# Performance work log

Measured on AMD Instinct MI355X. Metric: run time of the kernel, lower is better.

## Reference

```python
import jax, jax.numpy as jnp
import numpy as np

B, L, D, H = 2, 4096, 1024, 4
DK = D // H
DV = D // H
CHUNK, FIRS, FIRL, CONV, GROUP = 32, 3, 31, 4, 2
EPS_ID, R_EPS = 0.06, 0.025   # step==0 -> router epsilon at its start value
R_HID = 2 * D
R_IN = D + H * 6


def _l2norm(x, eps=1e-6):
    return x * jax.lax.rsqrt(jnp.sum(x * x, -1, keepdims=True) + eps)


def _causal_dwconv(x, w):
    # x: (b, l, c), w: (c, k); depthwise causal conv1d
    c = x.shape[-1]
    k = w.shape[-1]
    lhs = jnp.swapaxes(x, 1, 2)              # (b, c, l)
    rhs = w[:, None, :]                      # (c, 1, k)
    y = jax.lax.conv_general_dilated(lhs, rhs, window_strides=(1,), padding=[(k - 1, 0)],
                                     dimension_numbers=('NCH', 'OIH', 'NCH'), feature_group_count=c)
    return jnp.swapaxes(y, 1, 2)


def _fir(x, filt):
    # x: (b, l, h, d), filt: (h, d, k) depthwise causal FIR per head-channel
    b, l, h, d = x.shape
    y = _causal_dwconv(x.reshape(b, l, h * d), filt.reshape(h * d, -1))
    return y.reshape(b, l, h, d)


def _delta_rule_chunkwise(q, k, v, beta, chunk=CHUNK):
    # q,k: (b,h,L,dk)  v: (b,h,L,dv)  beta: (b,h,L); L % chunk == 0
    b, h, Ls, dk = q.shape
    dv = v.shape[-1]
    n = Ls // chunk
    q = _l2norm(q)
    k = _l2norm(k)
    v = v * beta[..., None]
    kb = k * beta[..., None]
    rs = lambda t: t.reshape(b, h, n, chunk, -1)
    q, k, v, kb = map(rs, (q, k, v, kb))
    tri = jnp.triu(jnp.ones((chunk, chunk), bool), 0)
    # UT transform: forward substitution to invert (I + strictly-lower(K_beta K^T))
    T = jnp.where(tri, 0.0, -(kb @ jnp.swapaxes(k, -1, -2)))
    for i in range(1, chunk):
        T = T.at[..., i, :].add(jnp.einsum('...j,...jl->...l', T[..., i, :], T))
    T = T + jnp.eye(chunk, dtype=T.dtype)
    u = T @ v          # (b,h,n,c,dv)
    w = T @ kb         # (b,h,n,c,dk)
    fmask = jnp.triu(jnp.ones((chunk, chunk), bool), 1)
    mv = lambda t: jnp.moveaxis(t, 2, 0)

    def step(S, xs):
        qi, ki, ui, wi = xs
        attn = jnp.where(fmask, 0.0, qi @ jnp.swapaxes(ki, -1, -2))
        u2 = ui - wi @ S
        oi = qi @ S + attn @ u2
        return S + jnp.swapaxes(ki, -1, -2) @ u2, oi

    S0 = jnp.zeros((b, h, dk, dv), q.dtype)
    S, o = jax.lax.scan(step, S0, (mv(q), mv(k), mv(u), mv(w)))
    return jnp.moveaxis(o, 0, 2).reshape(b, h, Ls, dv), S


def setup_inputs():
    key = jax.random.key(0)
    ks = jax.random.split(key, 20)
    lin = lambda kk, i, o: 0.02 * jax.random.normal(kk, (i, o), jnp.float32)

    def fir(kk, kern):
        base = jnp.zeros((H, DV, kern), jnp.float32).at[:, :, -1].set(1.0)
        return base + 0.01 * jax.random.normal(kk, (H, DV, kern), jnp.float32)

    return {
        'hidden_states': jax.random.normal(ks[0], (B, L, D), jnp.float32),
        'Wq': lin(ks[1], D, H * DK), 'Wk': lin(ks[2], D, H * DK), 'Wv': lin(ks[3], D, H * DV),
        'Wb': lin(ks[4], D, H),
        'conv_q': 0.3 * jax.random.normal(ks[5], (H * DK, CONV), jnp.float32),
        'conv_k': 0.3 * jax.random.normal(ks[6], (H * DK, CONV), jnp.float32),
        'conv_v': 0.3 * jax.random.normal(ks[7], (H * DV, CONV), jnp.float32),
        'fir_short': fir(ks[8], FIRS), 'fir_long': fir(ks[9], FIRL),
        'alpha_id': jnp.zeros((H,), jnp.float32),
        'Wid': lin(ks[10], D, H), 'bid': jnp.zeros((H,), jnp.float32),
        'Wr1': lin(ks[11], R_IN, R_HID), 'br1': jnp.zeros((R_HID,), jnp.float32),
        'Wr2': lin(ks[12], R_HID, H * 3), 'br2': jnp.zeros((H * 3,), jnp.float32),
        'log_tau_group': jnp.zeros(((H + GROUP - 1) // GROUP,), jnp.float32),
        'log_tau_head': jnp.zeros((H,), jnp.float32),
        'o_norm_w': jnp.ones((DV,), jnp.float32),
        'Wo': lin(ks[13], H * DV, D),
    }


def reference(hidden_states, Wq, Wk, Wv, Wb, conv_q, conv_k, conv_v, fir_short, fir_long,
              alpha_id, Wid, bid, Wr1, br1, Wr2, br2, log_tau_group, log_tau_head, o_norm_w, Wo):
    x = hidden_states
    b, l = x.shape[:2]
    # projections + causal short conv + silu (qk_activation='silu')
    q = jax.nn.silu(_causal_dwconv(x @ Wq, conv_q))
    k = jax.nn.silu(_causal_dwconv(x @ Wk, conv_k))
    v = jax.nn.silu(_causal_dwconv(x @ Wv, conv_v))
    qh = q.reshape(b, l, H, DK)
    kh = k.reshape(b, l, H, DK)
    vh = v.reshape(b, l, H, DV)
    beta = jax.nn.sigmoid(x @ Wb)                      # (b,l,h)
    bhld = lambda t: jnp.transpose(t, (0, 2, 1, 3))
    delta, _S = _delta_rule_chunkwise(bhld(qh), bhld(kh), bhld(vh), jnp.transpose(beta, (0, 2, 1)))
    delta = jnp.transpose(delta, (0, 2, 1, 3))         # (b,l,h,dv)
    fs = _fir(vh, fir_short)
    fl = _fir(vh, fir_long)
    # per-head mean/std stats of the three branch outputs
    stats = jnp.concatenate([fs.mean(-1), fs.std(-1), fl.mean(-1), fl.std(-1),
                             delta.mean(-1), delta.std(-1)], -1)   # (b,l,6h)
    router_in = jnp.concatenate([x, stats], -1)
    hmid = jax.nn.gelu(router_in @ Wr1 + br1, approximate=False)
    logits = (hmid @ Wr2 + br2).reshape(b, l, H, 3)
    group_idx = jnp.arange(H) // GROUP
    # step==0 -> mix=1.0: tau is the per-group temperature
    tau = jnp.exp(log_tau_group)[group_idx] + 0.0 * jnp.exp(log_tau_head)
    p = jax.nn.softmax(logits / tau[None, None, :, None], -1)
    p = p * (1.0 - 3.0 * R_EPS) + R_EPS                # epsilon-floor
    o = p[..., 0:1] * fs + p[..., 1:2] * fl + p[..., 2:3] * delta
    # gated identity (value) path
    id_scale = EPS_ID + jax.nn.sigmoid(alpha_id)[None, None, :] * jax.nn.sigmoid(x @ Wid + bid)
    o = o + id_scale[..., None] * vh
    # per-head RMSNorm then output projection
    o = o * jax.lax.rsqrt(jnp.mean(o * o, -1, keepdims=True) + 1e-5) * o_norm_w
    return o.reshape(b, l, H * DV) @ Wo
```

## Files before the change

### kernel.cpp

```cpp
#include <hip/hip_runtime.h>
#include <hip/hip_bf16.h>
#include <math.h>

#define BATCH 2
#define SEQ 4096
#define DMODEL 1024
#define NH 4
#define DHEAD 256
#define NCHUNK 128
#define ROWS (BATCH * SEQ)

typedef short s8v __attribute__((ext_vector_type(8)));
typedef float f4v __attribute__((ext_vector_type(4)));

__device__ __forceinline__ float sigm(float x) { return 1.0f / (1.0f + expf(-x)); }
__device__ __forceinline__ float siluf(float x) { return x / (1.0f + expf(-x)); }
__device__ __forceinline__ unsigned short f2b(float f) {
  __hip_bfloat16 h = __float2bfloat16(f);
  return *(unsigned short*)&h;
}
__device__ __forceinline__ float b2f(unsigned short u) {
  __hip_bfloat16 h = *(__hip_bfloat16*)&u;
  return __bfloat162float(h);
}
__device__ __forceinline__ unsigned int pk2(float lo, float hi) {
  return (unsigned int)f2b(lo) | ((unsigned int)f2b(hi) << 16);
}
__device__ __forceinline__ void gload16(const short* g, short* l) {
  __builtin_amdgcn_global_load_lds(
      (const __attribute__((address_space(1))) unsigned int*)(const void*)g,
      (__attribute__((address_space(3))) unsigned int*)(void*)l, 16, 0, 0);
}


__device__ __forceinline__ void prep_body(
    const float* __restrict__ x, __hip_bfloat16* __restrict__ xb,
    const float* __restrict__ Wb, const float* __restrict__ Wid,
    const float* __restrict__ alpha_id, const float* __restrict__ bidp,
    float* __restrict__ beta, float* __restrict__ idsc, int row,
    float (*red)[8]) {
  const int t = threadIdx.x;
  const long base = (long)row * DMODEL + t * 4;
  float4 xv = *(const float4*)(x + base);
  {
    __hip_bfloat16 tmp[4] = {__float2bfloat16(xv.x), __float2bfloat16(xv.y),
                             __float2bfloat16(xv.z), __float2bfloat16(xv.w)};
    *(ushort4*)(xb + base) = *(ushort4*)tmp;
  }
  float xa[4] = {xv.x, xv.y, xv.z, xv.w};
  float ab[4] = {0, 0, 0, 0}, ai[4] = {0, 0, 0, 0};
#pragma unroll
  for (int i = 0; i < 4; ++i) {
    int k = t * 4 + i;
    float4 wb4 = *(const float4*)(Wb + k * 4);
    float4 wi4 = *(const float4*)(Wid + k * 4);
    ab[0] = fmaf(xa[i], wb4.x, ab[0]); ab[1] = fmaf(xa[i], wb4.y, ab[1]);
    ab[2] = fmaf(xa[i], wb4.z, ab[2]); ab[3] = fmaf(xa[i], wb4.w, ab[3]);
    ai[0] = fmaf(xa[i], wi4.x, ai[0]); ai[1] = fmaf(xa[i], wi4.y, ai[1]);
    ai[2] = fmaf(xa[i], wi4.z, ai[2]); ai[3] = fmaf(xa[i], wi4.w, ai[3]);
  }
#pragma unroll
  for (int m = 1; m < 64; m <<= 1) {
#pragma unroll
    for (int hh = 0; hh < 4; ++hh) {
      ab[hh] += __shfl_xor(ab[hh], m);
      ai[hh] += __shfl_xor(ai[hh], m);
    }
  }
  if ((t & 63) == 0) {
    int wv = t >> 6;
#pragma unroll
    for (int hh = 0; hh < 4; ++hh) {
      red[wv][hh] = ab[hh];
      red[wv][4 + hh] = ai[hh];
    }
  }
  __syncthreads();
  if (t < 8) {
    float s = red[0][t] + red[1][t] + red[2][t] + red[3][t];
    if (t < 4) {
      beta[(long)row * NH + t] = sigm(s);
    } else {
      int hh = t - 4;
      idsc[(long)row * NH + hh] = 0.06f + sigm(alpha_id[hh]) * sigm(s + bidp[hh]);
    }
  }
}

__device__ __forceinline__ void tcast_body(
    const float* __restrict__ W, __hip_bfloat16* __restrict__ Wt,
    int K, int N, int Ks, int bx, int by, float (*tile)[33]) {
  const int t = threadIdx.x;
  const int tx = t & 31, ty = t >> 5;
  const int kb = by * 32, nb = bx * 32;
#pragma unroll
  for (int r = 0; r < 4; ++r) {
    int kk = kb + ty + 8 * r;
    tile[ty + 8 * r][tx] = (kk < K) ? W[(long)kk * N + nb + tx] : 0.f;
  }
  __syncthreads();
#pragma unroll
  for (int r = 0; r < 4; ++r) {
    Wt[(long)(nb + ty + 8 * r) * Ks + kb + tx] = __float2bfloat16(tile[tx][ty + 8 * r]);
  }
}

__device__ __forceinline__ void firT_body(
    const float* __restrict__ fshort, const float* __restrict__ flong,
    float* __restrict__ fsT, float* __restrict__ flT, int j) {
  const int t = threadIdx.x;
  if (j < 31) {
#pragma unroll
    for (int i = 0; i < 4; ++i) {
      int c = t * 4 + i;
      flT[j * 1024 + c] = flong[c * 31 + j];
    }
  } else {
    int tp = j - 31;
#pragma unroll
    for (int i = 0; i < 4; ++i) {
      int c = t * 4 + i;
      fsT[tp * 1024 + c] = fshort[c * 3 + tp];
    }
  }
}

__device__ __forceinline__ void stats_body(
    const float* __restrict__ x, const float* __restrict__ fs,
    const float* __restrict__ fl, const float* __restrict__ dl,
    __hip_bfloat16* __restrict__ rinb, int row) {
  const int b = row >> 12;
  const int l = row & (SEQ - 1);
  const int t = threadIdx.x;
  float4 xv = *(const float4*)(x + (long)row * DMODEL + t * 4);
  {
    __hip_bfloat16 tmp[4] = {__float2bfloat16(xv.x), __float2bfloat16(xv.y),
                             __float2bfloat16(xv.z), __float2bfloat16(xv.w)};
    *(ushort4*)(rinb + (long)row * 1056 + t * 4) = *(ushort4*)tmp;
  }
  if (t < 8) rinb[(long)row * 1056 + 1048 + t] = __float2bfloat16(0.f);
  const int h = t >> 6;
  const int lane = t & 63;
  const long base = (long)row * DMODEL + h * DHEAD + lane * 4;
  const long dbase = ((long)(b * NH + h) * SEQ + l) * DHEAD + lane * 4;
  float4 a = *(const float4*)(fs + base);
  float4 bq = *(const float4*)(fl + base);
  float4 cq = *(const float4*)(dl + dbase);
  float s[6];
  s[0] = a.x + a.y + a.z + a.w;
  s[1] = a.x * a.x + a.y * a.y + a.z * a.z + a.w * a.w;
  s[2] = bq.x + bq.y + bq.z + bq.w;
  s[3] = bq.x * bq.x + bq.y * bq.y + bq.z * bq.z + bq.w * bq.w;
  s[4] = cq.x + cq.y + cq.z + cq.w;
  s[5] = cq.x * cq.x + cq.y * cq.y + cq.z * cq.z + cq.w * cq.w;
#pragma unroll
  for (int m = 1; m < 64; m <<= 1)
#pragma unroll
    for (int j = 0; j < 6; ++j) s[j] += __shfl_xor(s[j], m);
  if (lane == 0) {
    __hip_bfloat16* rb = rinb + (long)row * 1056 + 1024;
    float m0 = s[0] * (1.f / 256.f);
    float m1 = s[2] * (1.f / 256.f);
    float m2 = s[4] * (1.f / 256.f);
    rb[h] = __float2bfloat16(m0);
    rb[4 + h] = __float2bfloat16(sqrtf(fmaxf(s[1] * (1.f / 256.f) - m0 * m0, 0.f)));
    rb[8 + h] = __float2bfloat16(m1);
    rb[12 + h] = __float2bfloat16(sqrtf(fmaxf(s[3] * (1.f / 256.f) - m1 * m1, 0.f)));
    rb[16 + h] = __float2bfloat16(m2);
    rb[20 + h] = __float2bfloat16(sqrtf(fmaxf(s[5] * (1.f / 256.f) - m2 * m2, 0.f)));
  }
}


__global__ __launch_bounds__(256) void head_fused(
    const float* __restrict__ x, __hip_bfloat16* __restrict__ xb,
    const float* __restrict__ Wb, const float* __restrict__ Wid,
    const float* __restrict__ alpha_id, const float* __restrict__ bidp,
    float* __restrict__ beta, float* __restrict__ idsc,
    const float* __restrict__ Wq, __hip_bfloat16* __restrict__ Wqt,
    const float* __restrict__ Wk, __hip_bfloat16* __restrict__ Wkt,
    const float* __restrict__ Wv, __hip_bfloat16* __restrict__ Wvt,
    const float* __restrict__ fir_s, const float* __restrict__ fir_l,
    float* __restrict__ fsT, float* __restrict__ flT) {
  __shared__ float tile[32][33];
  __shared__ float red[4][8];
  const int bid = blockIdx.x;
  if (bid < 8192) {
    prep_body(x, xb, Wb, Wid, alpha_id, bidp, beta, idsc, bid, red);
  } else if (bid < 9216) {
    int r = bid - 8192;
    tcast_body(Wq, Wqt, 1024, 1024, 1024, r & 31, r >> 5, tile);
  } else if (bid < 10240) {
    int r = bid - 9216;
    tcast_body(Wk, Wkt, 1024, 1024, 1024, r & 31, r >> 5, tile);
  } else if (bid < 11264) {
    int r = bid - 10240;
    tcast_body(Wv, Wvt, 1024, 1024, 1024, r & 31, r >> 5, tile);
  } else {
    firT_body(fir_s, fir_l, fsT, flT, bid - 11264);
  }
}

__global__ __launch_bounds__(256) void stats_tcast(
    const float* __restrict__ x, const float* __restrict__ fs,
    const float* __restrict__ fl, const float* __restrict__ dl,
    __hip_bfloat16* __restrict__ rinb,
    const float* __restrict__ Wr1, __hip_bfloat16* __restrict__ Wr1t,
    const float* __restrict__ Wo, __hip_bfloat16* __restrict__ Wot) {
  __shared__ float tile[32][33];
  const int bid = blockIdx.x;
  if (bid < 8192) {
    stats_body(x, fs, fl, dl, rinb, bid);
  } else if (bid < 10304) {
    int r = bid - 8192;
    tcast_body(Wr1, Wr1t, 1048, 2048, 1056, r & 63, r >> 6, tile);
  } else {
    int r = bid - 10304;
    tcast_body(Wo, Wot, 1024, 1024, 1024, r & 31, r >> 5, tile);
  }
}

template <int ACT, bool BF16OUT>
__global__ __launch_bounds__(256) void gemm_bf16(
    const __hip_bfloat16* __restrict__ A, const __hip_bfloat16* __restrict__ Bt,
    const float* __restrict__ bias, void* __restrict__ Cv,
    int M, int N, int Ks) {
  __shared__ short As[128 * 32];
  __shared__ short Bs[128 * 32];
  const int t = threadIdx.x;
  const int wv = t >> 6;
  const int lane = t & 63;
  const int row0 = blockIdx.y * 128, col0 = blockIdx.x * 128;
  const int mq = (wv >> 1) * 64, nq = (wv & 1) * 64;
  const int ln15 = lane & 15;
  const int kq = (lane >> 4) * 8;
  const int srow = wv * 16 + (lane >> 2);
  const int scol = (lane & 3) * 8;
  const short* Ag0 = (const short*)A + (long)(row0 + srow) * Ks + scol;
  const short* Ag1 = Ag0 + (long)64 * Ks;
  const short* Bg0 = (const short*)Bt + (long)(col0 + srow) * Ks + scol;
  const short* Bg1 = Bg0 + (long)64 * Ks;
  short* Ad0 = &As[(wv * 16) * 32];
  short* Ad1 = &As[(64 + wv * 16) * 32];
  short* Bd0 = &Bs[(wv * 16) * 32];
  short* Bd1 = &Bs[(64 + wv * 16) * 32];

  f4v acc[4][4];
#pragma unroll
  for (int i = 0; i < 4; ++i)
#pragma unroll
    for (int j = 0; j < 4; ++j) acc[i][j] = (f4v){0.f, 0.f, 0.f, 0.f};

  for (int k0 = 0; k0 < Ks; k0 += 32) {
    __syncthreads();
    gload16(Ag0 + k0, Ad0);
    gload16(Ag1 + k0, Ad1);
    gload16(Bg0 + k0, Bd0);
    gload16(Bg1 + k0, Bd1);
    __syncthreads();
    s8v af[4], bf[4];
#pragma unroll
    for (int mt = 0; mt < 4; ++mt)
      af[mt] = *(const s8v*)&As[(mq + mt * 16 + ln15) * 32 + kq];
#pragma unroll
    for (int nt = 0; nt < 4; ++nt)
      bf[nt] = *(const s8v*)&Bs[(nq + nt * 16 + ln15) * 32 + kq];
#pragma unroll
    for (int mt = 0; mt < 4; ++mt)
#pragma unroll
      for (int nt = 0; nt < 4; ++nt)
        acc[mt][nt] = __builtin_amdgcn_mfma_f32_16x16x32_bf16(af[mt], bf[nt], acc[mt][nt], 0, 0, 0);
  }
  const int rbase = (lane >> 4) * 4;
#pragma unroll
  for (int mt = 0; mt < 4; ++mt) {
#pragma unroll
    for (int nt = 0; nt < 4; ++nt) {
      int gcol = col0 + nq + nt * 16 + ln15;
#pragma unroll
      for (int r = 0; r < 4; ++r) {
        int grow = row0 + mq + mt * 16 + rbase + r;
        float v = acc[mt][nt][r];
        if (ACT == 1) {
          v += bias[gcol];
          v = 0.5f * v * (1.0f + erff(v * 0.70710678118654752f));
        }
        if (BF16OUT) {
          ((__hip_bfloat16*)Cv)[(long)grow * N + gcol] = __float2bfloat16(v);
        } else {
          ((float*)Cv)[(long)grow * N + gcol] = v;
        }
      }
    }
  }
}

template <int MODE>
__global__ __launch_bounds__(256) void conv_silu(
    const float* __restrict__ pre, const float* __restrict__ cw, float* __restrict__ out) {
  const int row = blockIdx.x;
  const int l = row & (SEQ - 1);
  const int t = threadIdx.x;
  const int cb = t * 4;
  float wts[4][4];
#pragma unroll
  for (int cc = 0; cc < 4; ++cc) {
    float4 w4 = *(const float4*)(cw + (cb + cc) * 4);
    wts[cc][0] = w4.x; wts[cc][1] = w4.y; wts[cc][2] = w4.z; wts[cc][3] = w4.w;
  }
  float acc[4] = {0, 0, 0, 0};
#pragma unroll
  for (int tap = 0; tap < 4; ++tap) {
    int lr = l - 3 + tap;
    if (lr >= 0) {
      float4 xv = *(const float4*)(pre + (long)(row - 3 + tap) * DMODEL + cb);
      acc[0] = fmaf(wts[0][tap], xv.x, acc[0]);
      acc[1] = fmaf(wts[1][tap], xv.y, acc[1]);
      acc[2] = fmaf(wts[2][tap], xv.z, acc[2]);
      acc[3] = fmaf(wts[3][tap], xv.w, acc[3]);
    }
  }
#pragma unroll
  for (int i = 0; i < 4; ++i) acc[i] = siluf(acc[i]);
  if (MODE == 1) {
    float ss = acc[0] * acc[0] + acc[1] * acc[1] + acc[2] * acc[2] + acc[3] * acc[3];
#pragma unroll
    for (int m = 1; m < 64; m <<= 1) ss += __shfl_xor(ss, m);
    float rn = rsqrtf(ss + 1e-6f);
#pragma unroll
    for (int i = 0; i < 4; ++i) acc[i] *= rn;
  }
  float4 ov = make_float4(acc[0], acc[1], acc[2], acc[3]);
  *(float4*)(out + (long)row * DMODEL + cb) = ov;
}

__global__ __launch_bounds__(256) void phaseA(
    const float* __restrict__ qn, const float* __restrict__ kn, const float* __restrict__ v,
    const float* __restrict__ beta, float* __restrict__ u,
    __hip_bfloat16* __restrict__ wb16, __hip_bfloat16* __restrict__ kTb16,
    __hip_bfloat16* __restrict__ attnb16, __hip_bfloat16* __restrict__ qpk) {
  __shared__ short khi[32 * 264];
  __shared__ short klo[32 * 264];
  __shared__ float T[32][33];
  __shared__ float bet[32];
  const int bid = blockIdx.x;
  const int c = bid & (NCHUNK - 1);
  const int h = (bid >> 7) & 3;
  const int b = bid >> 9;
  const int bh = b * NH + h;
  const int l0 = c * 32;
  const int t = threadIdx.x;
  const int wv = t >> 6;
  const int lane = t & 63;
  const int ln15 = lane & 15;
  const int qw = lane >> 4;

#pragma unroll
  for (int r = 0; r < 8; ++r) {
    int idx = t + 256 * r;
    int i = idx >> 6;
    int f = (idx & 63) * 4;
    float4 kv = *(const float4*)(kn + ((long)(b * SEQ + l0 + i)) * DMODEL + h * DHEAD + f);
    float a[4] = {kv.x, kv.y, kv.z, kv.w};
    ushort4 hi4, lo4;
    unsigned short* hp = (unsigned short*)&hi4;
    unsigned short* lp = (unsigned short*)&lo4;
#pragma unroll
    for (int j = 0; j < 4; ++j) {
      unsigned short hb = f2b(a[j]);
      hp[j] = hb;
      lp[j] = f2b(a[j] - b2f(hb));
    }
    *(ushort4*)&khi[i * 264 + f] = hi4;
    *(ushort4*)&klo[i * 264 + f] = lo4;
  }
  if (t < 32) bet[t] = beta[(long)(b * SEQ + l0 + t) * NH + h];
  __syncthreads();

  if (wv < 2) {
    const int mt = wv;
    f4v acc0 = (f4v){0.f, 0.f, 0.f, 0.f};
    f4v acc1 = (f4v){0.f, 0.f, 0.f, 0.f};
#pragma unroll
    for (int ks = 0; ks < 8; ++ks) {
      s8v ahi = *(const s8v*)&khi[(mt * 16 + ln15) * 264 + ks * 32 + qw * 8];
      s8v alo = *(const s8v*)&klo[(mt * 16 + ln15) * 264 + ks * 32 + qw * 8];
      s8v bhi0 = *(const s8v*)&khi[ln15 * 264 + ks * 32 + qw * 8];
      s8v blo0 = *(const s8v*)&klo[ln15 * 264 + ks * 32 + qw * 8];
      s8v bhi1 = *(const s8v*)&khi[(16 + ln15) * 264 + ks * 32 + qw * 8];
      s8v blo1 = *(const s8v*)&klo[(16 + ln15) * 264 + ks * 32 + qw * 8];
      acc0 = __builtin_amdgcn_mfma_f32_16x16x32_bf16(ahi, bhi0, acc0, 0, 0, 0);
      acc0 = __builtin_amdgcn_mfma_f32_16x16x32_bf16(ahi, blo0, acc0, 0, 0, 0);
      acc0 = __builtin_amdgcn_mfma_f32_16x16x32_bf16(alo, bhi0, acc0, 0, 0, 0);
      acc1 = __builtin_amdgcn_mfma_f32_16x16x32_bf16(ahi, bhi1, acc1, 0, 0, 0);
      acc1 = __builtin_amdgcn_mfma_f32_16x16x32_bf16(ahi, blo1, acc1, 0, 0, 0);
      acc1 = __builtin_amdgcn_mfma_f32_16x16x32_bf16(alo, bhi1, acc1, 0, 0, 0);
    }
#pragma unroll
    for (int r = 0; r < 4; ++r) {
      int i = mt * 16 + qw * 4 + r;
      int j0 = ln15, j1 = 16 + ln15;
      T[i][j0] = (j0 < i) ? -bet[i] * acc0[r] : 0.f;
      T[i][j1] = (j1 < i) ? -bet[i] * acc1[r] : 0.f;
    }
  } else {
    const int mt = wv - 2;
    const long qoff = (long)(b * SEQ + l0 + mt * 16 + ln15) * DMODEL + h * DHEAD;
    __hip_bfloat16* qdst = qpk + ((long)bh * SEQ + l0 + mt * 16 + ln15) * DHEAD;
    f4v acc0 = (f4v){0.f, 0.f, 0.f, 0.f};
    f4v acc1 = (f4v){0.f, 0.f, 0.f, 0.f};
#pragma unroll
    for (int ks = 0; ks < 8; ++ks) {
      float4 q0 = *(const float4*)(qn + qoff + ks * 32 + qw * 8);
      float4 q1 = *(const float4*)(qn + qoff + ks * 32 + qw * 8 + 4);
      float a8[8] = {q0.x, q0.y, q0.z, q0.w, q1.x, q1.y, q1.z, q1.w};
      s8v ahi, alo;
#pragma unroll
      for (int j = 0; j < 8; ++j) {
        unsigned short hb = f2b(a8[j]);
        ahi[j] = (short)hb;
        alo[j] = (short)f2b(a8[j] - b2f(hb));
      }
      *(s8v*)(qdst + ks * 32 + qw * 8) = ahi;
      s8v bhi0 = *(const s8v*)&khi[ln15 * 264 + ks * 32 + qw * 8];
      s8v blo0 = *(const s8v*)&klo[ln15 * 264 + ks * 32 + qw * 8];
      s8v bhi1 = *(const s8v*)&khi[(16 + ln15) * 264 + ks * 32 + qw * 8];
      s8v blo1 = *(const s8v*)&klo[(16 + ln15) * 264 + ks * 32 + qw * 8];
      acc0 = __builtin_amdgcn_mfma_f32_16x16x32_bf16(ahi, bhi0, acc0, 0, 0, 0);
      acc0 = __builtin_amdgcn_mfma_f32_16x16x32_bf16(ahi, blo0, acc0, 0, 0, 0);
      acc0 = __builtin_amdgcn_mfma_f32_16x16x32_bf16(alo, bhi0, acc0, 0, 0, 0);
      acc1 = __builtin_amdgcn_mfma_f32_16x16x32_bf16(ahi, bhi1, acc1, 0, 0, 0);
      acc1 = __builtin_amdgcn_mfma_f32_16x16x32_bf16(ahi, blo1, acc1, 0, 0, 0);
      acc1 = __builtin_amdgcn_mfma_f32_16x16x32_bf16(alo, bhi1, acc1, 0, 0, 0);
    }
    long abase = ((long)bh * NCHUNK + c) * 1024;
#pragma unroll
    for (int r = 0; r < 4; ++r) {
      int i = mt * 16 + qw * 4 + r;
      int j0 = ln15, j1 = 16 + ln15;
      attnb16[abase + i * 32 + j0] = __float2bfloat16(j0 <= i ? acc0[r] : 0.f);
      attnb16[abase + i * 32 + j1] = __float2bfloat16(j1 <= i ? acc1[r] : 0.f);
    }
  }
  __syncthreads();

  if (t < 32) {
    const int l = t;
    for (int i = 1; i < 32; ++i) {
      float s = 0.f;
      for (int j = 0; j < i; ++j) s = fmaf(T[i][j], T[j][l], s);
      T[i][l] += s;
    }
    for (int i = 0; i < 32; ++i) {
      float val = T[i][l] + (i == l ? 1.f : 0.f);
      T[i][l] = val * bet[l];
    }
  }
  __syncthreads();

  {
    const int d = t;
    float acc[32];
#pragma unroll
    for (int i = 0; i < 32; ++i) acc[i] = 0.f;
    for (int j = 0; j < 32; ++j) {
      float vv = v[((long)(b * SEQ + l0 + j)) * DMODEL + h * DHEAD + d];
#pragma unroll
      for (int i = 0; i < 32; ++i) acc[i] = fmaf(T[i][j], vv, acc[i]);
    }
    long ubase = ((long)bh * SEQ + l0) * DHEAD + d;
#pragma unroll
    for (int i = 0; i < 32; ++i) u[ubase + (long)i * DHEAD] = acc[i];
#pragma unroll
    for (int i = 0; i < 32; ++i) acc[i] = 0.f;
    for (int j = 0; j < 32; ++j) {
      float kv = b2f((unsigned short)khi[j * 264 + d]) + b2f((unsigned short)klo[j * 264 + d]);
#pragma unroll
      for (int i = 0; i < 32; ++i) acc[i] = fmaf(T[i][j], kv, acc[i]);
    }
#pragma unroll
    for (int i = 0; i < 32; ++i) wb16[ubase + (long)i * DHEAD] = __float2bfloat16(acc[i]);
  }

  {
    const int s = t;
    unsigned short* kb = (unsigned short*)kTb16 + ((long)bh * NCHUNK + c) * 8192 + (long)s * 32;
#pragma unroll
    for (int i4 = 0; i4 < 8; ++i4) {
      ushort4 pk;
      pk.x = (unsigned short)khi[(i4 * 4 + 0) * 264 + s];
      pk.y = (unsigned short)khi[(i4 * 4 + 1) * 264 + s];
      pk.z = (unsigned short)khi[(i4 * 4 + 2) * 264 + s];
      pk.w = (unsigned short)khi[(i4 * 4 + 3) * 264 + s];
      *(ushort4*)(kb + i4 * 4) = pk;
    }
  }
}

__global__ __launch_bounds__(64, 1) void phaseB(
    const __hip_bfloat16* __restrict__ qpk, const __hip_bfloat16* __restrict__ wb,
    const __hip_bfloat16* __restrict__ kTb, const __hip_bfloat16* __restrict__ attnb,
    const float* __restrict__ u, float* __restrict__ delta) {
  __shared__ __align__(16) short St[16 * 264];
  const int bid = blockIdx.x;
  const int slice = bid & 15;
  const int bh = bid >> 4;
  const int d0 = slice * 16;
  const int t = threadIdx.x;
  const int ln15 = t & 15;
  const int qw = t >> 4;

  const short* wbase = (const short*)wb + (long)bh * SEQ * 256;
  const short* qbase = (const short*)qpk + (long)bh * SEQ * 256;
  const short* kTbase = (const short*)kTb + (long)bh * NCHUNK * 8192;
  const short* atbase = (const short*)attnb + (long)bh * NCHUNK * 1024;
  const float* ubase = u + (long)bh * SEQ * 256;
  float* dbase = delta + (long)bh * SEQ * 256;

  f4v Sacc[16];
#pragma unroll
  for (int kt = 0; kt < 16; ++kt) Sacc[kt] = (f4v){0.f, 0.f, 0.f, 0.f};

  s8v wA[2][8], kA[16], atv[2];
  float uf[2][4];
  {
#pragma unroll
    for (int mt = 0; mt < 2; ++mt)
#pragma unroll
      for (int ks = 0; ks < 8; ++ks)
        wA[mt][ks] = *(const s8v*)(wbase + (long)(mt * 16 + ln15) * 256 + ks * 32 + qw * 8);
#pragma unroll
    for (int kt = 0; kt < 16; ++kt)
      kA[kt] = *(const s8v*)(kTbase + (kt * 16 + ln15) * 32 + qw * 8);
#pragma unroll
    for (int mt = 0; mt < 2; ++mt) {
      atv[mt] = *(const s8v*)(atbase + (mt * 16 + ln15) * 32 + qw * 8);
#pragma unroll
      for (int r = 0; r < 4; ++r)
        uf[mt][r] = ubase[(long)(mt * 16 + qw * 4 + r) * 256 + d0 + ln15];
    }
  }

  const int idx0 = (((qw & 1) * 2) * 16 + ln15) * 4;
  const int idx1 = (((qw & 1) * 2 + 1) * 16 + ln15) * 4;
  const bool hiHalf = (qw >= 2);

  s8v bS[8];
#pragma unroll
  for (int ks = 0; ks < 8; ++ks) bS[ks] = (s8v){0, 0, 0, 0, 0, 0, 0, 0};

  for (int c = 0; c < NCHUNK; ++c) {
    const int l0 = c * 32;

    s8v qA[2][8];
#pragma unroll
    for (int mt = 0; mt < 2; ++mt)
#pragma unroll
      for (int ks = 0; ks < 8; ++ks)
        qA[mt][ks] = *(const s8v*)(qbase + (long)(l0 + mt * 16 + ln15) * 256 + ks * 32 + qw * 8);

    f4v dwa0 = (f4v){0.f,0.f,0.f,0.f}, dwb0 = (f4v){0.f,0.f,0.f,0.f};
    f4v dwa1 = (f4v){0.f,0.f,0.f,0.f}, dwb1 = (f4v){0.f,0.f,0.f,0.f};
#pragma unroll
    for (int ks = 0; ks < 4; ++ks) {
      dwa0 = __builtin_amdgcn_mfma_f32_16x16x32_bf16(wA[0][ks], bS[ks], dwa0, 0, 0, 0);
      dwa1 = __builtin_amdgcn_mfma_f32_16x16x32_bf16(wA[1][ks], bS[ks], dwa1, 0, 0, 0);
      dwb0 = __builtin_amdgcn_mfma_f32_16x16x32_bf16(wA[0][ks + 4], bS[ks + 4], dwb0, 0, 0, 0);
      dwb1 = __builtin_amdgcn_mfma_f32_16x16x32_bf16(wA[1][ks + 4], bS[ks + 4], dwb1, 0, 0, 0);
    }
    float u2a[4], u2b[4];
#pragma unroll
    for (int r = 0; r < 4; ++r) {
      u2a[r] = uf[0][r] - (dwa0[r] + dwb0[r]);
      u2b[r] = uf[1][r] - (dwa1[r] + dwb1[r]);
    }
    s8v bu;
    {
      int A0 = (int)pk2(u2a[0], u2a[1]);
      int A1 = (int)pk2(u2a[2], u2a[3]);
      int B0 = (int)pk2(u2b[0], u2b[1]);
      int B1 = (int)pk2(u2b[2], u2b[3]);
      int p0a = __builtin_amdgcn_ds_bpermute(idx0, A0);
      int p0b = __builtin_amdgcn_ds_bpermute(idx0, B0);
      int p1a = __builtin_amdgcn_ds_bpermute(idx0, A1);
      int p1b = __builtin_amdgcn_ds_bpermute(idx0, B1);
      int p2a = __builtin_amdgcn_ds_bpermute(idx1, A0);
      int p2b = __builtin_amdgcn_ds_bpermute(idx1, B0);
      int p3a = __builtin_amdgcn_ds_bpermute(idx1, A1);
      int p3b = __builtin_amdgcn_ds_bpermute(idx1, B1);
      int4 buw = make_int4(hiHalf ? p0b : p0a, hiHalf ? p1b : p1a,
                           hiHalf ? p2b : p2a, hiHalf ? p3b : p3a);
      bu = *(s8v*)&buw;
    }

    f4v oA0 = __builtin_amdgcn_mfma_f32_16x16x32_bf16(atv[0], bu, (f4v){0.f,0.f,0.f,0.f}, 0, 0, 0);
    f4v oA1 = __builtin_amdgcn_mfma_f32_16x16x32_bf16(atv[1], bu, (f4v){0.f,0.f,0.f,0.f}, 0, 0, 0);

#pragma unroll
    for (int kt = 0; kt < 16; ++kt)
      Sacc[kt] = __builtin_amdgcn_mfma_f32_16x16x32_bf16(kA[kt], bu, Sacc[kt], 0, 0, 0);

    s8v bSn[8];
    if (c + 1 < NCHUNK) {
#pragma unroll
      for (int kt = 0; kt < 16; ++kt) {
        ushort4 pk;
        pk.x = f2b(Sacc[kt][0]); pk.y = f2b(Sacc[kt][1]);
        pk.z = f2b(Sacc[kt][2]); pk.w = f2b(Sacc[kt][3]);
        *(ushort4*)&St[ln15 * 264 + kt * 16 + qw * 4] = pk;
      }
#pragma unroll
      for (int ks = 0; ks < 8; ++ks)
        bSn[ks] = *(const s8v*)&St[ln15 * 264 + ks * 32 + qw * 8];

      const int ln = l0 + 32;
#pragma unroll
      for (int mt = 0; mt < 2; ++mt)
#pragma unroll
        for (int ks = 0; ks < 8; ++ks)
          wA[mt][ks] = *(const s8v*)(wbase + (long)(ln + mt * 16 + ln15) * 256 + ks * 32 + qw * 8);
#pragma unroll
      for (int kt = 0; kt < 16; ++kt)
        kA[kt] = *(const s8v*)(kTbase + (long)(c + 1) * 8192 + (kt * 16 + ln15) * 32 + qw * 8);
#pragma unroll
      for (int mt = 0; mt < 2; ++mt) {
        atv[mt] = *(const s8v*)(atbase + (long)(c + 1) * 1024 + (mt * 16 + ln15) * 32 + qw * 8);
#pragma unroll
        for (int r = 0; r < 4; ++r)
          uf[mt][r] = ubase[(long)(ln + mt * 16 + qw * 4 + r) * 256 + d0 + ln15];
      }
    }

    f4v oB0 = (f4v){0.f,0.f,0.f,0.f}, oB1 = (f4v){0.f,0.f,0.f,0.f};
#pragma unroll
    for (int ks = 0; ks < 4; ++ks) {
      oA0 = __builtin_amdgcn_mfma_f32_16x16x32_bf16(qA[0][ks], bS[ks], oA0, 0, 0, 0);
      oA1 = __builtin_amdgcn_mfma_f32_16x16x32_bf16(qA[1][ks], bS[ks], oA1, 0, 0, 0);
      oB0 = __builtin_amdgcn_mfma_f32_16x16x32_bf16(qA[0][ks + 4], bS[ks + 4], oB0, 0, 0, 0);
      oB1 = __builtin_amdgcn_mfma_f32_16x16x32_bf16(qA[1][ks + 4], bS[ks + 4], oB1, 0, 0, 0);
    }
#pragma unroll
    for (int r = 0; r < 4; ++r) {
      dbase[(long)(l0 + qw * 4 + r) * 256 + d0 + ln15] = oA0[r] + oB0[r];
      dbase[(long)(l0 + 16 + qw * 4 + r) * 256 + d0 + ln15] = oA1[r] + oB1[r];
    }
    if (c + 1 < NCHUNK) {
#pragma unroll
      for (int ks = 0; ks < 8; ++ks) bS[ks] = bSn[ks];
    }
  }
}

__global__ __launch_bounds__(256) void fir_kernel(
    const float* __restrict__ v, const float* __restrict__ fsT,
    const float* __restrict__ flT, float* __restrict__ fs, float* __restrict__ fl) {
  const int row = blockIdx.x;
  const int l = row & (SEQ - 1);
  const int t = threadIdx.x;
  const int cb = t * 4;
  float4 accl = make_float4(0, 0, 0, 0);
  float4 accs = make_float4(0, 0, 0, 0);
  const float* vb = v + (long)(row - 30) * DMODEL + cb;
  if (l >= 30) {
#pragma unroll
    for (int j = 0; j < 31; ++j) {
      float4 w4 = *(const float4*)(flT + j * DMODEL + cb);
      float4 xv = *(const float4*)(vb + (long)j * DMODEL);
      accl.x = fmaf(w4.x, xv.x, accl.x);
      accl.y = fmaf(w4.y, xv.y, accl.y);
      accl.z = fmaf(w4.z, xv.z, accl.z);
      accl.w = fmaf(w4.w, xv.w, accl.w);
      if (j >= 28) {
        float4 s4 = *(const float4*)(fsT + (j - 28) * DMODEL + cb);
        accs.x = fmaf(s4.x, xv.x, accs.x);
        accs.y = fmaf(s4.y, xv.y, accs.y);
        accs.z = fmaf(s4.z, xv.z, accs.z);
        accs.w = fmaf(s4.w, xv.w, accs.w);
      }
    }
  } else {
    for (int j = 30 - l; j < 31; ++j) {
      float4 w4 = *(const float4*)(flT + j * DMODEL + cb);
      float4 xv = *(const float4*)(vb + (long)j * DMODEL);
      accl.x = fmaf(w4.x, xv.x, accl.x);
      accl.y = fmaf(w4.y, xv.y, accl.y);
      accl.z = fmaf(w4.z, xv.z, accl.z);
      accl.w = fmaf(w4.w, xv.w, accl.w);
      if (j >= 28) {
        float4 s4 = *(const float4*)(fsT + (j - 28) * DMODEL + cb);
        accs.x = fmaf(s4.x, xv.x, accs.x);
        accs.y = fmaf(s4.y, xv.y, accs.y);
        accs.z = fmaf(s4.z, xv.z, accs.z);
        accs.w = fmaf(s4.w, xv.w, accs.w);
      }
    }
  }
  *(float4*)(fs + (long)row * DMODEL + cb) = accs;
  *(float4*)(fl + (long)row * DMODEL + cb) = accl;
}

__global__ __launch_bounds__(256) void router_logits(
    const __hip_bfloat16* __restrict__ hmid, const float* __restrict__ Wr2,
    const float* __restrict__ br2, const float* __restrict__ ltg, float* __restrict__ p) {
  const int row = blockIdx.x;
  const int t = threadIdx.x;
  float acc[12];
#pragma unroll
  for (int j = 0; j < 12; ++j) acc[j] = 0.f;
  const __hip_bfloat16* hr = hmid + (long)row * 2048;
  for (int k = t; k < 2048; k += 256) {
    float hv = __bfloat162float(hr[k]);
    const float* wr = Wr2 + k * 12;
#pragma unroll
    for (int j = 0; j < 12; ++j) acc[j] = fmaf(hv, wr[j], acc[j]);
  }
#pragma unroll
  for (int m = 1; m < 64; m <<= 1)
#pragma unroll
    for (int j = 0; j < 12; ++j) acc[j] += __shfl_xor(acc[j], m);
  __shared__ float red[4][12];
  if ((t & 63) == 0) {
    int wv = t >> 6;
#pragma unroll
    for (int j = 0; j < 12; ++j) red[wv][j] = acc[j];
  }
  __syncthreads();
  if (t < 4) {
    const int h = t;
    float l3[3];
#pragma unroll
    for (int j = 0; j < 3; ++j) {
      int col = h * 3 + j;
      l3[j] = red[0][col] + red[1][col] + red[2][col] + red[3][col] + br2[col];
    }
    float inv_tau = expf(-ltg[h >> 1]);
    float y0 = l3[0] * inv_tau, y1 = l3[1] * inv_tau, y2 = l3[2] * inv_tau;
    float mx = fmaxf(y0, fmaxf(y1, y2));
    float e0 = expf(y0 - mx), e1 = expf(y1 - mx), e2 = expf(y2 - mx);
    float inv = 1.f / (e0 + e1 + e2);
    p[(long)row * 12 + h * 3 + 0] = e0 * inv * 0.925f + 0.025f;
    p[(long)row * 12 + h * 3 + 1] = e1 * inv * 0.925f + 0.025f;
    p[(long)row * 12 + h * 3 + 2] = e2 * inv * 0.925f + 0.025f;
  }
}

__global__ __launch_bounds__(256) void omix(
    const float* __restrict__ fs, const float* __restrict__ fl,
    const float* __restrict__ dl, const float* __restrict__ vh,
    const float* __restrict__ p, const float* __restrict__ idsc,
    const float* __restrict__ onw, __hip_bfloat16* __restrict__ o) {
  const int row = blockIdx.x;
  const int b = row >> 12;
  const int l = row & (SEQ - 1);
  const int t = threadIdx.x;
  const int h = t >> 6;
  const int lane = t & 63;
  const long base = (long)row * DMODEL + h * DHEAD + lane * 4;
  const long dbase = ((long)(b * NH + h) * SEQ + l) * DHEAD + lane * 4;
  float p0 = p[(long)row * 12 + h * 3 + 0];
  float p1 = p[(long)row * 12 + h * 3 + 1];
  float p2 = p[(long)row * 12 + h * 3 + 2];
  float idv = idsc[(long)row * NH + h];
  float4 a = *(const float4*)(fs + base);
  float4 bq = *(const float4*)(fl + base);
  float4 cq = *(const float4*)(dl + dbase);
  float4 vv = *(const float4*)(vh + base);
  float4 ov;
  ov.x = p0 * a.x + p1 * bq.x + p2 * cq.x + idv * vv.x;
  ov.y = p0 * a.y + p1 * bq.y + p2 * cq.y + idv * vv.y;
  ov.z = p0 * a.z + p1 * bq.z + p2 * cq.z + idv * vv.z;
  ov.w = p0 * a.w + p1 * bq.w + p2 * cq.w + idv * vv.w;
  float ss = ov.x * ov.x + ov.y * ov.y + ov.z * ov.z + ov.w * ov.w;
#pragma unroll
  for (int m = 1; m < 64; m <<= 1) ss += __shfl_xor(ss, m);
  float rms = rsqrtf(ss * (1.f / 256.f) + 1e-5f);
  float4 wn = *(const float4*)(onw + lane * 4);
  __hip_bfloat16 tmp[4] = {__float2bfloat16(ov.x * rms * wn.x),
                           __float2bfloat16(ov.y * rms * wn.y),
                           __float2bfloat16(ov.z * rms * wn.z),
                           __float2bfloat16(ov.w * rms * wn.w)};
  *(ushort4*)(o + base) = *(ushort4*)tmp;
}

extern "C" void kernel_launch(void* const* d_in, const int* in_sizes, int n_in,
                              void* d_out, int out_size, void* d_ws, size_t ws_size,
                              hipStream_t stream) {
  const float* x = (const float*)d_in[0];
  const float* Wq = (const float*)d_in[1];
  const float* Wk = (const float*)d_in[2];
  const float* Wv = (const float*)d_in[3];
  const float* Wb = (const float*)d_in[4];
  const float* conv_q = (const float*)d_in[5];
  const float* conv_k = (const float*)d_in[6];
  const float* conv_v = (const float*)d_in[7];
  const float* fir_s = (const float*)d_in[8];
  const float* fir_l = (const float*)d_in[9];
  const float* alpha_id = (const float*)d_in[10];
  const float* Wid = (const float*)d_in[11];
  const float* bidp = (const float*)d_in[12];
  const float* Wr1 = (const float*)d_in[13];
  const float* br1 = (const float*)d_in[14];
  const float* Wr2 = (const float*)d_in[15];
  const float* br2 = (const float*)d_in[16];
  const float* ltg = (const float*)d_in[17];
  const float* onw = (const float*)d_in[19];
  const float* Wo = (const float*)d_in[20];

  float* ws = (float*)d_ws;
  float* pre = ws + 0;
  float* ubuf = ws + 8388608;
  float* wbuf = ws + 16777216;
  float* attnbuf = ws + 25165824;
  float* qbuf = ws + 26214400;
  float* kbuf = ws + 34603008;
  float* vbuf = ws + 42991616;
  float* betabuf = ws + 51380224;
  float* idscbuf = ws + 51412992;
  float* pbuf = ws + 51445760;
  float* flTb = ws + 51544064;
  float* fsTb = ws + 51575808;
  float* deltabuf = ubuf;
  __hip_bfloat16* xb = (__hip_bfloat16*)ubuf;
  __hip_bfloat16* Wqt = (__hip_bfloat16*)(wbuf);
  __hip_bfloat16* Wkt = (__hip_bfloat16*)(wbuf + 524288);
  __hip_bfloat16* Wvt = (__hip_bfloat16*)(wbuf + 1048576);
  __hip_bfloat16* wb16 = (__hip_bfloat16*)wbuf;
  __hip_bfloat16* kTb16 = (__hip_bfloat16*)wbuf + 8388608;
  __hip_bfloat16* attnb16 = (__hip_bfloat16*)attnbuf;
  __hip_bfloat16* qpk16 = (__hip_bfloat16*)pre;
  __hip_bfloat16* rinb = (__hip_bfloat16*)(wbuf);
  __hip_bfloat16* Wr1t = (__hip_bfloat16*)(wbuf + 4325376);
  __hip_bfloat16* Wot = (__hip_bfloat16*)(wbuf + 5406720);
  __hip_bfloat16* omixb = (__hip_bfloat16*)(wbuf);
  __hip_bfloat16* hmid = (__hip_bfloat16*)pre;
  float* fsb = qbuf;
  float* flb = kbuf;

  dim3 blk(256);
  head_fused<<<dim3(11298), blk, 0, stream>>>(x, xb, Wb, Wid, alpha_id, bidp,
      betabuf, idscbuf, Wq, Wqt, Wk, Wkt, Wv, Wvt, fir_s, fir_l, fsTb, flTb);
  gemm_bf16<0, false><<<dim3(8, 64), blk, 0, stream>>>(xb, Wqt, nullptr, pre, ROWS, 1024, 1024);
  conv_silu<1><<<dim3(ROWS), blk, 0, stream>>>(pre, conv_q, qbuf);
  gemm_bf16<0, false><<<dim3(8, 64), blk, 0, stream>>>(xb, Wkt, nullptr, pre, ROWS, 1024, 1024);
  conv_silu<1><<<dim3(ROWS), blk, 0, stream>>>(pre, conv_k, kbuf);
  gemm_bf16<0, false><<<dim3(8, 64), blk, 0, stream>>>(xb, Wvt, nullptr, pre, ROWS, 1024, 1024);
  conv_silu<0><<<dim3(ROWS), blk, 0, stream>>>(pre, conv_v, vbuf);
  phaseA<<<dim3(BATCH * NH * NCHUNK), blk, 0, stream>>>(qbuf, kbuf, vbuf, betabuf, ubuf, wb16, kTb16, attnb16, qpk16);
  phaseB<<<dim3(BATCH * NH * 16), dim3(64), 0, stream>>>(qpk16, wb16, kTb16, attnb16, ubuf, deltabuf);
  fir_kernel<<<dim3(ROWS), blk, 0, stream>>>(vbuf, fsTb, flTb, fsb, flb);
  stats_tcast<<<dim3(11328), blk, 0, stream>>>(x, fsb, flb, deltabuf, rinb, Wr1, Wr1t, Wo, Wot);
  gemm_bf16<1, true><<<dim3(16, 64), blk, 0, stream>>>(rinb, Wr1t, br1, hmid, ROWS, 2048, 1056);
  router_logits<<<dim3(ROWS), blk, 0, stream>>>(hmid, Wr2, br2, ltg, pbuf);
  omix<<<dim3(ROWS), blk, 0, stream>>>(fsb, flb, deltabuf, vbuf, pbuf, idscbuf, onw, omixb);
  gemm_bf16<0, false><<<dim3(8, 64), blk, 0, stream>>>(omixb, Wot, nullptr, d_out, ROWS, 1024, 1024);
}
```

Baseline: 903.8 us.

## Tile FIR with shared-memory sliding window, swizzle GEMM blocks, restructure phaseB exchanges

The per-row FIR kernel is replaced by a tiled version. It stages a 62-row window of v in shared memory, keeps the filter taps in registers and slides a register window across 16 outputs per thread, which removes the repeated global reads of v and the filter. The GEMM remaps block indices so that consecutive blocks are spread in an XCD-friendly order, aiming at better L2 locality. In phaseB, the ds_bpermute exchange of u2 is replaced by an LDS round-trip through a small Ut buffer, and the S-to-bf16 transpose moves to the top of each chunk instead of being prefetched. That puts the transpose on the serial critical path and could slow the recurrence.

```diff
diff --git a/kernel.cpp b/kernel.cpp
--- a/kernel.cpp
+++ b/kernel.cpp
@@ -22,9 +22,6 @@
 __device__ __forceinline__ float b2f(unsigned short u) {
   __hip_bfloat16 h = *(__hip_bfloat16*)&u;
   return __bfloat162float(h);
-}
-__device__ __forceinline__ unsigned int pk2(float lo, float hi) {
-  return (unsigned int)f2b(lo) | ((unsigned int)f2b(hi) << 16);
 }
 __device__ __forceinline__ void gload16(const short* g, short* l) {
   __builtin_amdgcn_global_load_lds(
@@ -230,7 +227,11 @@
   const int t = threadIdx.x;
   const int wv = t >> 6;
   const int lane = t & 63;
-  const int row0 = blockIdx.y * 128, col0 = blockIdx.x * 128;
+  const int nx = gridDim.x;
+  int flat = blockIdx.y * nx + blockIdx.x;
+  const int q8 = (nx * gridDim.y) >> 3;
+  flat = (flat & 7) * q8 + (flat >> 3);
+  const int row0 = (flat / nx) * 128, col0 = (flat % nx) * 128;
   const int mq = (wv >> 1) * 64, nq = (wv & 1) * 64;
   const int ln15 = lane & 15;
   const int kq = (lane >> 4) * 8;
@@ -502,6 +503,7 @@
     const __hip_bfloat16* __restrict__ kTb, const __hip_bfloat16* __restrict__ attnb,
     const float* __restrict__ u, float* __restrict__ delta) {
   __shared__ __align__(16) short St[16 * 264];
+  __shared__ __align__(16) short Ut[16 * 40];
   const int bid = blockIdx.x;
   const int slice = bid & 15;
   const int bh = bid >> 4;
@@ -541,14 +543,6 @@
     }
   }
 
-  const int idx0 = (((qw & 1) * 2) * 16 + ln15) * 4;
-  const int idx1 = (((qw & 1) * 2 + 1) * 16 + ln15) * 4;
-  const bool hiHalf = (qw >= 2);
-
-  s8v bS[8];
-#pragma unroll
-  for (int ks = 0; ks < 8; ++ks) bS[ks] = (s8v){0, 0, 0, 0, 0, 0, 0, 0};
-
   for (int c = 0; c < NCHUNK; ++c) {
     const int l0 = c * 32;
 
@@ -558,6 +552,19 @@
 #pragma unroll
       for (int ks = 0; ks < 8; ++ks)
         qA[mt][ks] = *(const s8v*)(qbase + (long)(l0 + mt * 16 + ln15) * 256 + ks * 32 + qw * 8);
+
+#pragma unroll
+    for (int kt = 0; kt < 16; ++kt) {
+      ushort4 pk;
+      pk.x = f2b(Sacc[kt][0]); pk.y = f2b(Sacc[kt][1]);
+      pk.z = f2b(Sacc[kt][2]); pk.w = f2b(Sacc[kt][3]);
+      *(ushort4*)&St[ln15 * 264 + kt * 16 + qw * 4] = pk;
+    }
+    asm volatile("s_waitcnt lgkmcnt(0)" ::: "memory");
+    s8v bS[8];
+#pragma unroll
+    for (int ks = 0; ks < 8; ++ks)
+      bS[ks] = *(const s8v*)&St[ln15 * 264 + ks * 32 + qw * 8];
 
     f4v dwa0 = (f4v){0.f,0.f,0.f,0.f}, dwb0 = (f4v){0.f,0.f,0.f,0.f};
     f4v dwa1 = (f4v){0.f,0.f,0.f,0.f}, dwb1 = (f4v){0.f,0.f,0.f,0.f};
@@ -574,24 +581,15 @@
       u2a[r] = uf[0][r] - (dwa0[r] + dwb0[r]);
       u2b[r] = uf[1][r] - (dwa1[r] + dwb1[r]);
     }
-    s8v bu;
     {
-      int A0 = (int)pk2(u2a[0], u2a[1]);
-      int A1 = (int)pk2(u2a[2], u2a[3]);
-      int B0 = (int)pk2(u2b[0], u2b[1]);
-      int B1 = (int)pk2(u2b[2], u2b[3]);
-      int p0a = __builtin_amdgcn_ds_bpermute(idx0, A0);
-      int p0b = __builtin_amdgcn_ds_bpermute(idx0, B0);
-      int p1a = __builtin_amdgcn_ds_bpermute(idx0, A1);
-      int p1b = __builtin_amdgcn_ds_bpermute(idx0, B1);
-      int p2a = __builtin_amdgcn_ds_bpermute(idx1, A0);
-      int p2b = __builtin_amdgcn_ds_bpermute(idx1, B0);
-      int p3a = __builtin_amdgcn_ds_bpermute(idx1, A1);
-      int p3b = __builtin_amdgcn_ds_bpermute(idx1, B1);
-      int4 buw = make_int4(hiHalf ? p0b : p0a, hiHalf ? p1b : p1a,
-                           hiHalf ? p2b : p2a, hiHalf ? p3b : p3a);
-      bu = *(s8v*)&buw;
-    }
+      ushort4 pa, pb;
+      pa.x = f2b(u2a[0]); pa.y = f2b(u2a[1]); pa.z = f2b(u2a[2]); pa.w = f2b(u2a[3]);
+      pb.x = f2b(u2b[0]); pb.y = f2b(u2b[1]); pb.z = f2b(u2b[2]); pb.w = f2b(u2b[3]);
+      *(ushort4*)&Ut[(d0 * 0 + (t & 15)) * 40 + qw * 4] = pa;
+      *(ushort4*)&Ut[(t & 15) * 40 + 16 + qw * 4] = pb;
+    }
+    asm volatile("s_waitcnt lgkmcnt(0)" ::: "memory");
+    s8v bu = *(const s8v*)&Ut[ln15 * 40 + qw * 8];
 
     f4v oA0 = __builtin_amdgcn_mfma_f32_16x16x32_bf16(atv[0], bu, (f4v){0.f,0.f,0.f,0.f}, 0, 0, 0);
     f4v oA1 = __builtin_amdgcn_mfma_f32_16x16x32_bf16(atv[1], bu, (f4v){0.f,0.f,0.f,0.f}, 0, 0, 0);
@@ -600,19 +598,7 @@
     for (int kt = 0; kt < 16; ++kt)
       Sacc[kt] = __builtin_amdgcn_mfma_f32_16x16x32_bf16(kA[kt], bu, Sacc[kt], 0, 0, 0);
 
-    s8v bSn[8];
     if (c + 1 < NCHUNK) {
-#pragma unroll
-      for (int kt = 0; kt < 16; ++kt) {
-        ushort4 pk;
-        pk.x = f2b(Sacc[kt][0]); pk.y = f2b(Sacc[kt][1]);
-        pk.z = f2b(Sacc[kt][2]); pk.w = f2b(Sacc[kt][3]);
-        *(ushort4*)&St[ln15 * 264 + kt * 16 + qw * 4] = pk;
-      }
-#pragma unroll
-      for (int ks = 0; ks < 8; ++ks)
-        bSn[ks] = *(const s8v*)&St[ln15 * 264 + ks * 32 + qw * 8];
-
       const int ln = l0 + 32;
 #pragma unroll
       for (int mt = 0; mt < 2; ++mt)
@@ -644,59 +630,57 @@
       dbase[(long)(l0 + qw * 4 + r) * 256 + d0 + ln15] = oA0[r] + oB0[r];
       dbase[(long)(l0 + 16 + qw * 4 + r) * 256 + d0 + ln15] = oA1[r] + oB1[r];
     }
-    if (c + 1 < NCHUNK) {
-#pragma unroll
-      for (int ks = 0; ks < 8; ++ks) bS[ks] = bSn[ks];
-    }
-  }
-}
-
-__global__ __launch_bounds__(256) void fir_kernel(
+  }
+}
+
+__global__ __launch_bounds__(256) void fir_tiled(
     const float* __restrict__ v, const float* __restrict__ fsT,
     const float* __restrict__ flT, float* __restrict__ fs, float* __restrict__ fl) {
-  const int row = blockIdx.x;
-  const int l = row & (SEQ - 1);
-  const int t = threadIdx.x;
-  const int cb = t * 4;
-  float4 accl = make_float4(0, 0, 0, 0);
-  float4 accs = make_float4(0, 0, 0, 0);
-  const float* vb = v + (long)(row - 30) * DMODEL + cb;
-  if (l >= 30) {
-#pragma unroll
-    for (int j = 0; j < 31; ++j) {
-      float4 w4 = *(const float4*)(flT + j * DMODEL + cb);
-      float4 xv = *(const float4*)(vb + (long)j * DMODEL);
-      accl.x = fmaf(w4.x, xv.x, accl.x);
-      accl.y = fmaf(w4.y, xv.y, accl.y);
-      accl.z = fmaf(w4.z, xv.z, accl.z);
-      accl.w = fmaf(w4.w, xv.w, accl.w);
-      if (j >= 28) {
-        float4 s4 = *(const float4*)(fsT + (j - 28) * DMODEL + cb);
-        accs.x = fmaf(s4.x, xv.x, accs.x);
-        accs.y = fmaf(s4.y, xv.y, accs.y);
-        accs.z = fmaf(s4.z, xv.z, accs.z);
-        accs.w = fmaf(s4.w, xv.w, accs.w);
-      }
-    }
-  } else {
-    for (int j = 30 - l; j < 31; ++j) {
-      float4 w4 = *(const float4*)(flT + j * DMODEL + cb);
-      float4 xv = *(const float4*)(vb + (long)j * DMODEL);
-      accl.x = fmaf(w4.x, xv.x, accl.x);
-      accl.y = fmaf(w4.y, xv.y, accl.y);
-      accl.z = fmaf(w4.z, xv.z, accl.z);
-      accl.w = fmaf(w4.w, xv.w, accl.w);
-      if (j >= 28) {
-        float4 s4 = *(const float4*)(fsT + (j - 28) * DMODEL + cb);
-        accs.x = fmaf(s4.x, xv.x, accs.x);
-        accs.y = fmaf(s4.y, xv.y, accs.y);
-        accs.z = fmaf(s4.z, xv.z, accs.z);
-        accs.w = fmaf(s4.w, xv.w, accs.w);
-      }
-    }
-  }
-  *(float4*)(fs + (long)row * DMODEL + cb) = accs;
-  *(float4*)(fl + (long)row * DMODEL + cb) = accl;
+  __shared__ float vt[62][128];
+  const int tile = blockIdx.x;
+  const int cg0 = blockIdx.y * 128;
+  const int t = threadIdx.x;
+  const int l0 = (tile * 32) & (SEQ - 1);
+  const long grow0 = (long)tile * 32;
+#pragma unroll
+  for (int i = 0; i < 8; ++i) {
+    int e = t + 256 * i;
+    int r = e >> 5, c4 = (e & 31) * 4;
+    if (r < 62) {
+      int lr = l0 - 30 + r;
+      float4 val = (lr >= 0)
+          ? *(const float4*)(v + (grow0 - 30 + r) * DMODEL + cg0 + c4)
+          : make_float4(0.f, 0.f, 0.f, 0.f);
+      *(float4*)&vt[r][c4] = val;
+    }
+  }
+  const int c = t & 127;
+  const int half = t >> 7;
+  float wl[31], wsv[3];
+#pragma unroll
+  for (int j = 0; j < 31; ++j) wl[j] = flT[j * DMODEL + cg0 + c];
+#pragma unroll
+  for (int j = 0; j < 3; ++j) wsv[j] = fsT[j * DMODEL + cg0 + c];
+  __syncthreads();
+  const int rb = half * 16;
+  float w[31];
+#pragma unroll
+  for (int j = 0; j < 31; ++j) w[j] = vt[rb + j][c];
+#pragma unroll
+  for (int i = 0; i < 16; ++i) {
+    float al = 0.f;
+#pragma unroll
+    for (int j = 0; j < 31; ++j) al = fmaf(wl[j], w[j], al);
+    float as = fmaf(wsv[2], w[30], fmaf(wsv[1], w[29], fmaf(wsv[0], w[28], 0.f)));
+    long orow = grow0 + rb + i;
+    fl[orow * DMODEL + cg0 + c] = al;
+    fs[orow * DMODEL + cg0 + c] = as;
+    if (i < 15) {
+#pragma unroll
+      for (int j = 0; j < 30; ++j) w[j] = w[j + 1];
+      w[30] = vt[rb + i + 31][c];
+    }
+  }
 }
 
 __global__ __launch_bounds__(256) void router_logits(
@@ -847,7 +831,7 @@
   conv_silu<0><<<dim3(ROWS), blk, 0, stream>>>(pre, conv_v, vbuf);
   phaseA<<<dim3(BATCH * NH * NCHUNK), blk, 0, stream>>>(qbuf, kbuf, vbuf, betabuf, ubuf, wb16, kTb16, attnb16, qpk16);
   phaseB<<<dim3(BATCH * NH * 16), dim3(64), 0, stream>>>(qpk16, wb16, kTb16, attnb16, ubuf, deltabuf);
-  fir_kernel<<<dim3(ROWS), blk, 0, stream>>>(vbuf, fsTb, flTb, fsb, flb);
+  fir_tiled<<<dim3(ROWS / 32, 8), blk, 0, stream>>>(vbuf, fsTb, flTb, fsb, flb);
   stats_tcast<<<dim3(11328), blk, 0, stream>>>(x, fsb, flb, deltabuf, rinb, Wr1, Wr1t, Wo, Wot);
   gemm_bf16<1, true><<<dim3(16, 64), blk, 0, stream>>>(rinb, Wr1t, br1, hmid, ROWS, 2048, 1056);
   router_logits<<<dim3(ROWS), blk, 0, stream>>>(hmid, Wr2, br2, ltg, pbuf);
```

New measurement: 805.6 us. 10.9% less time.
